# Optimization experiments

Hardware: AMD Instinct MI355X
Metric: run time of the kernel (lower is better)

Reference implementation:

```python
import jax, jax.numpy as jnp
import numpy as np

EPS = 1e-7  # K.epsilon()
ROUTINGS = 3
NUM_CAPSULE = 32
DIM_CAPSULE = 64


def squash(x, axis=-1):
    # NOTE: faithful to the source: x / sqrt(sum(x^2) + eps) (no squash factor)
    s = jnp.sum(jnp.square(x), axis=axis, keepdims=True)
    return x / jnp.sqrt(s + EPS)


def setup_inputs() -> dict:
    key = jax.random.key(0)
    k1, k2 = jax.random.split(key)
    B, I, C = 32, 1024, 256
    u_vecs = jax.random.normal(k1, (B, I, C), dtype=jnp.float32)
    # glorot-ish scale for the capsule kernel (1x1 conv == matmul C -> N*D)
    W = jax.random.normal(k2, (C, NUM_CAPSULE * DIM_CAPSULE), dtype=jnp.float32) * 0.03
    return {"u_vecs": u_vecs, "W": W}


def reference(u_vecs, W):
    B, I, C = u_vecs.shape
    N, D = NUM_CAPSULE, DIM_CAPSULE
    # conv1d with kernel size 1 == matmul; reshape + permute to (B, N, I, D)
    u_hat = jnp.einsum('bic,ce->bie', u_vecs, W)  # (B, I, N*D)
    u_hat = u_hat.reshape(B, I, N, D).transpose(0, 2, 1, 3)  # (B, N, I, D)

    b = jnp.zeros((B, N, I), dtype=u_hat.dtype)
    outputs = None
    for i in range(ROUTINGS):
        c = jax.nn.softmax(b, axis=1)  # softmax over num_capsule axis
        outputs = squash(jnp.einsum('bni,bnid->bnd', c, u_hat))  # (B, N, D)
        if i < ROUTINGS - 1:
            b = jnp.einsum('bnd,bnid->bni', outputs, u_hat)
    return outputs
```

## Files before the change

kernel.cpp:

```cpp
#include <hip/hip_runtime.h>
#include <math.h>


constexpr int Bn = 32, In = 1024, Cn = 256, Nn = 32, Dn = 64, ND = 2048;

typedef __attribute__((ext_vector_type(8))) short bf16x8;
typedef __attribute__((ext_vector_type(4))) float f32x4;

__device__ __forceinline__ unsigned int packbf2(float a, float b) {
  unsigned int xa = __float_as_uint(a), xb = __float_as_uint(b);
  xa = (xa + 0x7fffu + ((xa >> 16) & 1u)) >> 16;
  xb = (xb + 0x7fffu + ((xb >> 16) & 1u)) >> 16;
  return xa | (xb << 16);
}
__device__ __forceinline__ unsigned short packbf1(float a) {
  unsigned int x = __float_as_uint(a);
  return (unsigned short)((x + 0x7fffu + ((x >> 16) & 1u)) >> 16);
}
__device__ __forceinline__ float bfu(unsigned short us) {
  return __uint_as_float((unsigned int)us << 16);
}

__global__ __launch_bounds__(256) void k_pre(
    const float* __restrict__ u, const float* __restrict__ W,
    float* __restrict__ psu, unsigned short* __restrict__ Wbf,
    unsigned short* __restrict__ WbfT, unsigned short* __restrict__ ub16) {
  const int z = blockIdx.x, tid = threadIdx.x;
  if (z < 1024) {
    int b = z >> 5, ch = z & 31;
    const float* up = u + ((size_t)(b * In + ch * 32)) * Cn + tid;
    unsigned short* ubp = ub16 + ((size_t)(b * In + ch * 32)) * Cn + tid;
    float s = 0.f;
#pragma unroll 8
    for (int j = 0; j < 32; ++j) {
      float v = up[(size_t)j * Cn];
      s += v;
      ubp[(size_t)j * Cn] = packbf1(v);
    }
    psu[(size_t)z * Cn + tid] = s;
  } else if (z < 1152) {
    __shared__ float tile[64][65];
    int t = z - 1024;
    int x0 = (t & 31) * 64, y0 = (t >> 5) * 64;
    int lx = tid & 63, ly = tid >> 6;
#pragma unroll
    for (int k = 0; k < 16; ++k) {
      int y = ly + k * 4;
      tile[y][lx] = W[(size_t)(y0 + y) * ND + x0 + lx];
    }
    __syncthreads();
#pragma unroll
    for (int k = 0; k < 8; ++k) {
      int idx = tid + k * 256;
      int row = idx >> 5, cu = idx & 31;
      unsigned int v = packbf2(tile[2 * cu][row], tile[2 * cu + 1][row]);
      *(unsigned int*)&WbfT[(size_t)(x0 + row) * Cn + y0 + 2 * cu] = v;
    }
  } else {
    int zb = z - 1152;
    const float* src = W + (size_t)zb * 4096;
    unsigned short* dst = Wbf + (size_t)zb * 4096;
#pragma unroll
    for (int k = 0; k < 4; ++k) {
      int off = k * 1024 + tid * 4;
      const float4 v = *(const float4*)&src[off];
      *(uint2*)&dst[off] = make_uint2(packbf2(v.x, v.y), packbf2(v.z, v.w));
    }
  }
}

__global__ __launch_bounds__(256) void k_sst(
    const void* __restrict__ src, int srcBf16, int count, long bS, long nS,
    long cS, float scale, const unsigned short* __restrict__ Wbf,
    const unsigned short* __restrict__ WbfT, float* __restrict__ tb,
    float* __restrict__ outp, int writeT) {
  int bn = blockIdx.x, b = bn >> 5, n = bn & 31;
  int tid = threadIdx.x;
  __shared__ float vs[Cn];
  __shared__ float red[Cn];
  __shared__ float ol[Dn];
  {
    float s = 0.f;
    if (srcBf16) {
      const unsigned short* p = (const unsigned short*)src + b * bS + n * nS + tid;
      for (int ch = 0; ch < count; ++ch) s += bfu(p[(size_t)ch * cS]);
    } else {
      const float* p = (const float*)src + b * bS + n * nS + tid;
      for (int ch = 0; ch < count; ++ch) s += p[(size_t)ch * cS];
    }
    vs[tid] = s * scale;
  }
  __syncthreads();
  {
    int q = tid >> 6, d = tid & 63;
    const unsigned short* wp = Wbf + (size_t)(q * 64) * ND + (size_t)n * Dn + d;
    float a = 0.f;
#pragma unroll 8
    for (int c2 = 0; c2 < 64; ++c2) a += vs[q * 64 + c2] * bfu(wp[(size_t)c2 * ND]);
    red[tid] = a;
  }
  __syncthreads();
  if (tid < 64) {
    float a = red[tid] + red[64 + tid] + red[128 + tid] + red[192 + tid];
    float sq = a * a;
#pragma unroll
    for (int off = 32; off > 0; off >>= 1) sq += __shfl_xor(sq, off, 64);
    float o = a / sqrtf(sq + 1e-7f);
    ol[tid] = o;
    if (outp) outp[(size_t)bn * Dn + tid] = o;
  }
  __syncthreads();
  if (writeT) {
    const unsigned short* wt = WbfT + (size_t)(n * Dn) * Cn + tid;
    float a = 0.f;
#pragma unroll 8
    for (int d2 = 0; d2 < 64; ++d2) a += ol[d2] * bfu(wt[(size_t)d2 * Cn]);
    tb[(size_t)bn * Cn + tid] = a;
  }
}

__global__ __launch_bounds__(256, 4) void k_route(
    const float* __restrict__ tb, const unsigned short* __restrict__ ub16,
    unsigned short* __restrict__ pvb) {
  const int b = blockIdx.x, itile = blockIdx.y, i0 = itile * 32;
  const int tid = threadIdx.x;
  const int lane = tid & 63, w = tid >> 6;
  const int mrow = lane & 15, quad = lane >> 4;

  __shared__ unsigned short t_l[32][264];
  __shared__ unsigned short u_t[256][40];
  __shared__ unsigned short cm_l[32][40];
  __shared__ float bb_l[32][36];

  {
    const float* tp = tb + (size_t)b * Nn * Cn;
#pragma unroll
    for (int k = 0; k < 8; ++k) {
      int idx = tid + k * 256;
      int row = idx >> 6, q = idx & 63;
      const float4 tv = *(const float4*)&tp[(size_t)row * Cn + q * 4];
      *(uint2*)&t_l[row][q * 4] =
          make_uint2(packbf2(tv.x, tv.y), packbf2(tv.z, tv.w));
    }
    const int ti = tid & 31, qb = tid >> 5;
    const unsigned short* up = ub16 + ((size_t)(b * In + i0 + ti)) * Cn;
#pragma unroll
    for (int m = 0; m < 4; ++m) {
      int c8 = qb + m * 8;
      union { bf16x8 v; unsigned short us[8]; } uv;
      uv.v = *(const bf16x8*)&up[c8 * 8];
#pragma unroll
      for (int e = 0; e < 8; ++e) u_t[c8 * 8 + e][ti] = uv.us[e];
    }
  }
  __syncthreads();

  {
    const int i0t = (w & 1) * 16, n0t = (w >> 1) * 16;
    const unsigned short* ubp =
        ub16 + ((size_t)(b * In + i0 + i0t + mrow)) * Cn + quad * 8;
    f32x4 acc = {0.f, 0.f, 0.f, 0.f};
#pragma unroll
    for (int k0 = 0; k0 < 8; ++k0) {
      const bf16x8 af = *(const bf16x8*)(ubp + k0 * 32);
      const bf16x8 bf = *(const bf16x8*)&t_l[n0t + mrow][k0 * 32 + quad * 8];
      acc = __builtin_amdgcn_mfma_f32_16x16x32_bf16(af, bf, acc, 0, 0, 0);
    }
#pragma unroll
    for (int r = 0; r < 4; ++r)
      bb_l[n0t + mrow][i0t + quad * 4 + r] = acc[r];
  }
  __syncthreads();

  if (tid < 32) {
    float m = -1e30f;
#pragma unroll
    for (int n = 0; n < Nn; ++n) m = fmaxf(m, bb_l[n][tid]);
    float e[Nn];
    float ssum = 0.f;
#pragma unroll
    for (int n = 0; n < Nn; ++n) { e[n] = __expf(bb_l[n][tid] - m); ssum += e[n]; }
    float inv = 1.f / ssum;
#pragma unroll
    for (int n = 0; n < Nn; ++n) bb_l[n][tid] = e[n] * inv;
  }
  __syncthreads();

  {
    int n = tid >> 3, q = tid & 7;
    const float4 cv = *(const float4*)&bb_l[n][q * 4];
    *(uint2*)&cm_l[n][q * 4] = make_uint2(packbf2(cv.x, cv.y), packbf2(cv.z, cv.w));
  }
  __syncthreads();

  {
    const int mt = w & 1;
    const bf16x8 af = *(const bf16x8*)&cm_l[mt * 16 + mrow][quad * 8];
#pragma unroll
    for (int j = 0; j < 8; ++j) {
      const int ct = (w >> 1) * 8 + j;
      const bf16x8 bf = *(const bf16x8*)&u_t[ct * 16 + mrow][quad * 8];
      f32x4 d = {0.f, 0.f, 0.f, 0.f};
      d = __builtin_amdgcn_mfma_f32_16x16x32_bf16(af, bf, d, 0, 0, 0);
#pragma unroll
      for (int r = 0; r < 4; ++r)
        pvb[((size_t)((b * 32 + itile) * Nn + mt * 16 + quad * 4 + r)) * Cn +
            ct * 16 + mrow] = packbf1(d[r]);
    }
  }
}

extern "C" void kernel_launch(void* const* d_in, const int* in_sizes, int n_in,
                              void* d_out, int out_size, void* d_ws, size_t ws_size,
                              hipStream_t stream) {
  (void)in_sizes; (void)n_in; (void)out_size; (void)ws_size;
  const float* u = (const float*)d_in[0];
  const float* W = (const float*)d_in[1];
  float* out = (float*)d_out;
  float* ws = (float*)d_ws;
  unsigned short* pvb  = (unsigned short*)ws;
  float*          psu  = ws + 4194304;
  unsigned short* Wbf  = (unsigned short*)(ws + 4456448);
  unsigned short* WbfT = (unsigned short*)(ws + 4718592);
  float*          tbb  = ws + 4980736;
  unsigned short* ub16 = (unsigned short*)(ws + 5242880);

  k_pre<<<1280, 256, 0, stream>>>(u, W, psu, Wbf, WbfT, ub16);
  k_sst<<<1024, 256, 0, stream>>>(psu, 0, 32, 8192L, 0L, 256L, 1.0f / 32.0f,
                                  Wbf, WbfT, tbb, nullptr, 1);
  k_route<<<dim3(32, 32), 256, 0, stream>>>(tbb, ub16, pvb);
  k_sst<<<1024, 256, 0, stream>>>(pvb, 1, 32, 262144L, 256L, 8192L, 1.0f,
                                  Wbf, WbfT, tbb, nullptr, 1);
  k_route<<<dim3(32, 32), 256, 0, stream>>>(tbb, ub16, pvb);
  k_sst<<<1024, 256, 0, stream>>>(pvb, 1, 32, 262144L, 256L, 8192L, 1.0f,
                                  Wbf, WbfT, tbb, out, 0);
}
```

Measured before the change: 154.0 us.

## Vectorize k_sst loads, store tb as bf16, parallelize softmax, coalesce pvb stores

Result: faster. 126.8 us (-17.7%).

```diff
diff --git a/kernel.cpp b/kernel.cpp
--- a/kernel.cpp
+++ b/kernel.cpp
@@ -70,38 +70,78 @@
 }
 
 __global__ __launch_bounds__(256) void k_sst(
-    const void* __restrict__ src, int srcBf16, int count, long bS, long nS,
-    long cS, float scale, const unsigned short* __restrict__ Wbf,
-    const unsigned short* __restrict__ WbfT, float* __restrict__ tb,
+    const void* __restrict__ src, int srcBf16, long bS, long nS, long cS,
+    float scale, const unsigned short* __restrict__ Wbf,
+    const unsigned short* __restrict__ WbfT, unsigned short* __restrict__ tb,
     float* __restrict__ outp, int writeT) {
   int bn = blockIdx.x, b = bn >> 5, n = bn & 31;
   int tid = threadIdx.x;
   __shared__ float vs[Cn];
-  __shared__ float red[Cn];
   __shared__ float ol[Dn];
+  __shared__ float scr[2176];
+  {
+    const int g = tid >> 5, co = tid & 31;
+    float acc[8];
+#pragma unroll
+    for (int e = 0; e < 8; ++e) acc[e] = 0.f;
+    if (srcBf16) {
+      const unsigned short* p =
+          (const unsigned short*)src + b * bS + n * nS + co * 8;
+#pragma unroll
+      for (int k = 0; k < 4; ++k) {
+        union { bf16x8 v; unsigned short us[8]; } w;
+        w.v = *(const bf16x8*)&p[(size_t)(g * 4 + k) * cS];
+#pragma unroll
+        for (int e = 0; e < 8; ++e) acc[e] += bfu(w.us[e]);
+      }
+    } else {
+      const float* p = (const float*)src + b * bS + n * nS + co * 8;
+#pragma unroll
+      for (int k = 0; k < 4; ++k) {
+        const float4 v0 = *(const float4*)&p[(size_t)(g * 4 + k) * cS];
+        const float4 v1 = *(const float4*)&p[(size_t)(g * 4 + k) * cS + 4];
+        acc[0] += v0.x; acc[1] += v0.y; acc[2] += v0.z; acc[3] += v0.w;
+        acc[4] += v1.x; acc[5] += v1.y; acc[6] += v1.z; acc[7] += v1.w;
+      }
+    }
+    *(float4*)&scr[g * 272 + co * 8] =
+        make_float4(acc[0], acc[1], acc[2], acc[3]);
+    *(float4*)&scr[g * 272 + co * 8 + 4] =
+        make_float4(acc[4], acc[5], acc[6], acc[7]);
+  }
+  __syncthreads();
   {
     float s = 0.f;
-    if (srcBf16) {
-      const unsigned short* p = (const unsigned short*)src + b * bS + n * nS + tid;
-      for (int ch = 0; ch < count; ++ch) s += bfu(p[(size_t)ch * cS]);
-    } else {
-      const float* p = (const float*)src + b * bS + n * nS + tid;
-      for (int ch = 0; ch < count; ++ch) s += p[(size_t)ch * cS];
-    }
+#pragma unroll
+    for (int k = 0; k < 8; ++k) s += scr[k * 272 + tid];
     vs[tid] = s * scale;
   }
   __syncthreads();
   {
-    int q = tid >> 6, d = tid & 63;
-    const unsigned short* wp = Wbf + (size_t)(q * 64) * ND + (size_t)n * Dn + d;
+    const int cg = tid >> 3, do8 = tid & 7;
+    const unsigned short* wp =
+        Wbf + (size_t)(cg * 8) * ND + (size_t)n * Dn + do8 * 8;
+    float acc[8];
+#pragma unroll
+    for (int e = 0; e < 8; ++e) acc[e] = 0.f;
+#pragma unroll
+    for (int j = 0; j < 8; ++j) {
+      union { bf16x8 v; unsigned short us[8]; } w;
+      w.v = *(const bf16x8*)&wp[(size_t)j * ND];
+      const float vc = vs[cg * 8 + j];
+#pragma unroll
+      for (int e = 0; e < 8; ++e) acc[e] += vc * bfu(w.us[e]);
+    }
+    *(float4*)&scr[cg * 68 + do8 * 8] =
+        make_float4(acc[0], acc[1], acc[2], acc[3]);
+    *(float4*)&scr[cg * 68 + do8 * 8 + 4] =
+        make_float4(acc[4], acc[5], acc[6], acc[7]);
+  }
+  __syncthreads();
+  if (tid < 64) {
     float a = 0.f;
-#pragma unroll 8
-    for (int c2 = 0; c2 < 64; ++c2) a += vs[q * 64 + c2] * bfu(wp[(size_t)c2 * ND]);
-    red[tid] = a;
-  }
-  __syncthreads();
-  if (tid < 64) {
-    float a = red[tid] + red[64 + tid] + red[128 + tid] + red[192 + tid];
+#pragma unroll
+    for (int k = 0; k < 32; ++k) a += scr[k * 68 + tid];
     float sq = a * a;
 #pragma unroll
     for (int off = 32; off > 0; off >>= 1) sq += __shfl_xor(sq, off, 64);
@@ -111,16 +151,39 @@
   }
   __syncthreads();
   if (writeT) {
-    const unsigned short* wt = WbfT + (size_t)(n * Dn) * Cn + tid;
-    float a = 0.f;
-#pragma unroll 8
-    for (int d2 = 0; d2 < 64; ++d2) a += ol[d2] * bfu(wt[(size_t)d2 * Cn]);
-    tb[(size_t)bn * Cn + tid] = a;
+    {
+      const int dg = tid >> 5, co = tid & 31;
+      const unsigned short* wt =
+          WbfT + (size_t)(n * Dn + dg * 8) * Cn + co * 8;
+      float acc[8];
+#pragma unroll
+      for (int e = 0; e < 8; ++e) acc[e] = 0.f;
+#pragma unroll
+      for (int e = 0; e < 8; ++e) {
+        union { bf16x8 v; unsigned short us[8]; } w;
+        w.v = *(const bf16x8*)&wt[(size_t)e * Cn];
+        const float od = ol[dg * 8 + e];
+#pragma unroll
+        for (int cc = 0; cc < 8; ++cc) acc[cc] += od * bfu(w.us[cc]);
+      }
+      *(float4*)&scr[dg * 272 + co * 8] =
+          make_float4(acc[0], acc[1], acc[2], acc[3]);
+      *(float4*)&scr[dg * 272 + co * 8 + 4] =
+          make_float4(acc[4], acc[5], acc[6], acc[7]);
+    }
+    __syncthreads();
+    {
+      float s = 0.f;
+#pragma unroll
+      for (int k = 0; k < 8; ++k) s += scr[k * 272 + tid];
+      tb[(size_t)bn * Cn + tid] = packbf1(s);
+    }
   }
 }
 
 __global__ __launch_bounds__(256, 4) void k_route(
-    const float* __restrict__ tb, const unsigned short* __restrict__ ub16,
+    const unsigned short* __restrict__ tbb,
+    const unsigned short* __restrict__ ub16,
     unsigned short* __restrict__ pvb) {
   const int b = blockIdx.x, itile = blockIdx.y, i0 = itile * 32;
   const int tid = threadIdx.x;
@@ -131,16 +194,15 @@
   __shared__ unsigned short u_t[256][40];
   __shared__ unsigned short cm_l[32][40];
   __shared__ float bb_l[32][36];
-
-  {
-    const float* tp = tb + (size_t)b * Nn * Cn;
+  __shared__ float smr[2][8][32];
+
+  {
+    const unsigned short* tp = tbb + (size_t)b * Nn * Cn;
 #pragma unroll
     for (int k = 0; k < 8; ++k) {
       int idx = tid + k * 256;
       int row = idx >> 6, q = idx & 63;
-      const float4 tv = *(const float4*)&tp[(size_t)row * Cn + q * 4];
-      *(uint2*)&t_l[row][q * 4] =
-          make_uint2(packbf2(tv.x, tv.y), packbf2(tv.z, tv.w));
+      *(uint2*)&t_l[row][q * 4] = *(const uint2*)&tp[(size_t)row * Cn + q * 4];
     }
     const int ti = tid & 31, qb = tid >> 5;
     const unsigned short* up = ub16 + ((size_t)(b * In + i0 + ti)) * Cn;
@@ -172,17 +234,32 @@
   }
   __syncthreads();
 
-  if (tid < 32) {
-    float m = -1e30f;
-#pragma unroll
-    for (int n = 0; n < Nn; ++n) m = fmaxf(m, bb_l[n][tid]);
-    float e[Nn];
-    float ssum = 0.f;
-#pragma unroll
-    for (int n = 0; n < Nn; ++n) { e[n] = __expf(bb_l[n][tid] - m); ssum += e[n]; }
-    float inv = 1.f / ssum;
-#pragma unroll
-    for (int n = 0; n < Nn; ++n) bb_l[n][tid] = e[n] * inv;
+  {
+    const int i = tid & 31, g = tid >> 5;
+    float m4 = bb_l[g * 4 + 0][i];
+    m4 = fmaxf(m4, bb_l[g * 4 + 1][i]);
+    m4 = fmaxf(m4, bb_l[g * 4 + 2][i]);
+    m4 = fmaxf(m4, bb_l[g * 4 + 3][i]);
+    smr[0][g][i] = m4;
+    __syncthreads();
+    float m = smr[0][0][i];
+#pragma unroll
+    for (int k = 1; k < 8; ++k) m = fmaxf(m, smr[0][k][i]);
+    float s4 = 0.f;
+#pragma unroll
+    for (int r = 0; r < 4; ++r) {
+      float e = __expf(bb_l[g * 4 + r][i] - m);
+      bb_l[g * 4 + r][i] = e;
+      s4 += e;
+    }
+    smr[1][g][i] = s4;
+    __syncthreads();
+    float ss = 0.f;
+#pragma unroll
+    for (int k = 0; k < 8; ++k) ss += smr[1][k][i];
+    float inv = 1.f / ss;
+#pragma unroll
+    for (int r = 0; r < 4; ++r) bb_l[g * 4 + r][i] *= inv;
   }
   __syncthreads();
 
@@ -193,19 +270,31 @@
   }
   __syncthreads();
 
+  unsigned short* pvs = &t_l[0][0];
   {
     const int mt = w & 1;
     const bf16x8 af = *(const bf16x8*)&cm_l[mt * 16 + mrow][quad * 8];
 #pragma unroll
     for (int j = 0; j < 8; ++j) {
       const int ct = (w >> 1) * 8 + j;
-      const bf16x8 bf = *(const bf16x8*)&u_t[ct * 16 + mrow][quad * 8];
+      const bf16x8 bfv = *(const bf16x8*)&u_t[ct * 16 + mrow][quad * 8];
       f32x4 d = {0.f, 0.f, 0.f, 0.f};
-      d = __builtin_amdgcn_mfma_f32_16x16x32_bf16(af, bf, d, 0, 0, 0);
+      d = __builtin_amdgcn_mfma_f32_16x16x32_bf16(af, bfv, d, 0, 0, 0);
 #pragma unroll
       for (int r = 0; r < 4; ++r)
-        pvb[((size_t)((b * 32 + itile) * Nn + mt * 16 + quad * 4 + r)) * Cn +
-            ct * 16 + mrow] = packbf1(d[r]);
+        pvs[(size_t)(mt * 16 + quad * 4 + r) * 264 + ct * 16 + mrow] =
+            packbf1(d[r]);
+    }
+  }
+  __syncthreads();
+  {
+    unsigned short* pb = pvb + (size_t)((b * 32 + itile) * Nn) * Cn;
+    const int rg = tid >> 5, co = tid & 31;
+#pragma unroll
+    for (int k = 0; k < 4; ++k) {
+      int row = rg + k * 8;
+      const uint4 v = *(const uint4*)&pvs[(size_t)row * 264 + co * 8];
+      *(uint4*)&pb[(size_t)row * Cn + co * 8] = v;
     }
   }
 }
@@ -222,16 +311,16 @@
   float*          psu  = ws + 4194304;
   unsigned short* Wbf  = (unsigned short*)(ws + 4456448);
   unsigned short* WbfT = (unsigned short*)(ws + 4718592);
-  float*          tbb  = ws + 4980736;
+  unsigned short* tb16 = (unsigned short*)(ws + 4980736);
   unsigned short* ub16 = (unsigned short*)(ws + 5242880);
 
   k_pre<<<1280, 256, 0, stream>>>(u, W, psu, Wbf, WbfT, ub16);
-  k_sst<<<1024, 256, 0, stream>>>(psu, 0, 32, 8192L, 0L, 256L, 1.0f / 32.0f,
-                                  Wbf, WbfT, tbb, nullptr, 1);
-  k_route<<<dim3(32, 32), 256, 0, stream>>>(tbb, ub16, pvb);
-  k_sst<<<1024, 256, 0, stream>>>(pvb, 1, 32, 262144L, 256L, 8192L, 1.0f,
-                                  Wbf, WbfT, tbb, nullptr, 1);
-  k_route<<<dim3(32, 32), 256, 0, stream>>>(tbb, ub16, pvb);
-  k_sst<<<1024, 256, 0, stream>>>(pvb, 1, 32, 262144L, 256L, 8192L, 1.0f,
-                                  Wbf, WbfT, tbb, out, 0);
-}
+  k_sst<<<1024, 256, 0, stream>>>(psu, 0, 8192L, 0L, 256L, 1.0f / 32.0f,
+                                  Wbf, WbfT, tb16, nullptr, 1);
+  k_route<<<dim3(32, 32), 256, 0, stream>>>(tb16, ub16, pvb);
+  k_sst<<<1024, 256, 0, stream>>>(pvb, 1, 262144L, 256L, 8192L, 1.0f,
+                                  Wbf, WbfT, tb16, nullptr, 1);
+  k_route<<<dim3(32, 32), 256, 0, stream>>>(tb16, ub16, pvb);
+  k_sst<<<1024, 256, 0, stream>>>(pvb, 1, 262144L, 256L, 8192L, 1.0f,
+                                  Wbf, WbfT, tb16, out, 0);
+}
```
